# Kernel tuning notes

Measured on AMD Instinct MI355X. Metric: run time of the kernel, lower is better.

The kernel has to match this reference:

```python
import jax, jax.numpy as jnp
import numpy as np

N_NODES = 100_000
N_EDGES = 1_600_000
D_IN, D_HID, D_OUT = 256, 64, 32
NUM_PROP = 10
ALPHA = 0.1


def setup_inputs() -> dict:
    key = jax.random.key(0)
    ks = jax.random.split(key, 8)
    features = jax.random.normal(ks[0], (N_NODES, D_IN), dtype=jnp.float32)
    row = jax.random.randint(ks[1], (N_EDGES,), 0, N_NODES, dtype=jnp.int32)
    col = jax.random.randint(ks[2], (N_EDGES,), 0, N_NODES, dtype=jnp.int32)
    # positive edge weights (stand-in for symmetric-normalized adjacency values)
    edge_vals = jax.random.uniform(ks[3], (N_EDGES,), dtype=jnp.float32) / 16.0
    W1 = jax.random.normal(ks[4], (D_IN, D_HID), dtype=jnp.float32) / np.sqrt(D_IN)
    b1 = jnp.zeros((D_HID,), dtype=jnp.float32)
    W2 = jax.random.normal(ks[5], (D_HID, D_OUT), dtype=jnp.float32) / np.sqrt(D_HID)
    b2 = jnp.zeros((D_OUT,), dtype=jnp.float32)
    return {"features": features, "row": row, "col": col, "edge_vals": edge_vals,
            "W1": W1, "b1": b1, "W2": W2, "b2": b2}


def _spmm(row, col, vals, x):
    # COO sparse-dense matmul: out[r] += vals[e] * x[col[e]] for each edge e
    return jax.ops.segment_sum(vals[:, None] * x[col], row, num_segments=N_NODES)


def reference(features, row, col, edge_vals, W1, b1, W2, b2):
    # head_transform: 2-layer MLP
    x = jax.nn.relu(features @ W1 + b1) @ W2 + b2  # [N, D_OUT]
    x0 = x
    # APPNP propagation: x = (1-alpha) * (A @ x) + alpha * x0
    def body(_, x):
        return (1.0 - ALPHA) * _spmm(row, col, edge_vals, x) + ALPHA * x0
    x = jax.lax.fori_loop(0, NUM_PROP, body, x)
    return x
```

## Files before the change

kernel.cpp:

```cpp
#include <hip/hip_runtime.h>

#define N_NODES 100000
#define N_EDGES 1600000
#define D_IN    256
#define D_HID   64
#define D_OUT   32
#define NPROP   10

#define NBUCK 196
#define CHUNK 6080
#define NCHUNK ((N_EDGES + CHUNK - 1) / CHUNK)

typedef _Float16 half_t;
typedef _Float16 h8  __attribute__((ext_vector_type(8)));
typedef _Float16 h4  __attribute__((ext_vector_type(4)));
typedef float    f4v __attribute__((ext_vector_type(4)));

__global__ __launch_bounds__(256) void pack_kernel(
    const float* __restrict__ W1, const float* __restrict__ W2,
    half_t* __restrict__ W1T, half_t* __restrict__ W2T)
{
  int t = blockIdx.x * 256 + threadIdx.x;
  if (t < 64 * 256) { int n = t >> 8, k = t & 255; W1T[t] = (half_t)W1[k * 64 + n]; }
  if (t < 32 * 64)  { int n = t >> 6, k = t & 63;  W2T[t] = (half_t)W2[k * 32 + n]; }
}

#define HSTRIDE 72

__global__ __launch_bounds__(256, 4) void mlp_kernel(
    const float* __restrict__ F, const half_t* __restrict__ W1T,
    const float* __restrict__ b1, const half_t* __restrict__ W2T,
    const float* __restrict__ b2, half_t* __restrict__ x0h)
{
  __shared__ half_t h_lds[4 * 16 * HSTRIDE];
  __shared__ half_t out_lds[4 * 16 * 32];
  int t = threadIdx.x;
  int w = t >> 6, lane = t & 63;
  int m = lane & 15, q = lane >> 4;
  int gw = blockIdx.x * 4 + w;
  int node0 = gw * 16;
  if (node0 > N_NODES - 16) node0 = N_NODES - 16;

  f4v acc[4];
#pragma unroll
  for (int i = 0; i < 4; ++i) acc[i] = (f4v){0.f, 0.f, 0.f, 0.f};

  const float* ap = F + (size_t)(node0 + m) * D_IN + q * 8;

#pragma unroll
  for (int h = 0; h < 2; ++h) {
    h8 af[4];
#pragma unroll
    for (int s = 0; s < 4; ++s) {
      float4 f0 = *(const float4*)(ap + h * 128 + s * 32);
      float4 f1 = *(const float4*)(ap + h * 128 + s * 32 + 4);
      h8 a;
      a[0] = (_Float16)f0.x; a[1] = (_Float16)f0.y;
      a[2] = (_Float16)f0.z; a[3] = (_Float16)f0.w;
      a[4] = (_Float16)f1.x; a[5] = (_Float16)f1.y;
      a[6] = (_Float16)f1.z; a[7] = (_Float16)f1.w;
      af[s] = a;
    }
    const half_t* bp = W1T + (size_t)m * D_IN + h * 128 + q * 8;
#pragma unroll
    for (int s = 0; s < 4; ++s) {
      h8 b0 = *(const h8*)(bp + 0 * 16 * D_IN + s * 32);
      h8 b1v = *(const h8*)(bp + 1 * 16 * D_IN + s * 32);
      h8 b2v = *(const h8*)(bp + 2 * 16 * D_IN + s * 32);
      h8 b3v = *(const h8*)(bp + 3 * 16 * D_IN + s * 32);
      acc[0] = __builtin_amdgcn_mfma_f32_16x16x32_f16(af[s], b0, acc[0], 0, 0, 0);
      acc[1] = __builtin_amdgcn_mfma_f32_16x16x32_f16(af[s], b1v, acc[1], 0, 0, 0);
      acc[2] = __builtin_amdgcn_mfma_f32_16x16x32_f16(af[s], b2v, acc[2], 0, 0, 0);
      acc[3] = __builtin_amdgcn_mfma_f32_16x16x32_f16(af[s], b3v, acc[3], 0, 0, 0);
    }
  }

  half_t* hw = h_lds + w * 16 * HSTRIDE;
#pragma unroll
  for (int ht = 0; ht < 4; ++ht) {
    float bb = b1[ht * 16 + m];
#pragma unroll
    for (int i = 0; i < 4; ++i) {
      float hv = fmaxf(acc[ht][i] + bb, 0.f);
      hw[(q * 4 + i) * HSTRIDE + ht * 16 + m] = (half_t)hv;
    }
  }
  __syncthreads();

  f4v o0 = {0.f, 0.f, 0.f, 0.f}, o1 = {0.f, 0.f, 0.f, 0.f};
#pragma unroll
  for (int s = 0; s < 2; ++s) {
    h8 a = *(const h8*)(hw + m * HSTRIDE + s * 32 + q * 8);
    h8 bb0 = *(const h8*)(W2T + (size_t)m * D_HID + s * 32 + q * 8);
    h8 bb1 = *(const h8*)(W2T + (size_t)(16 + m) * D_HID + s * 32 + q * 8);
    o0 = __builtin_amdgcn_mfma_f32_16x16x32_f16(a, bb0, o0, 0, 0, 0);
    o1 = __builtin_amdgcn_mfma_f32_16x16x32_f16(a, bb1, o1, 0, 0, 0);
  }
  half_t* ow = out_lds + w * 16 * 32;
  {
    float c0 = b2[m], c1 = b2[16 + m];
#pragma unroll
    for (int i = 0; i < 4; ++i) {
      ow[(q * 4 + i) * 32 + m]      = (half_t)(o0[i] + c0);
      ow[(q * 4 + i) * 32 + 16 + m] = (half_t)(o1[i] + c1);
    }
  }
  __syncthreads();

  {
    int nl = lane >> 2, qq = lane & 3;
    *(int4*)(x0h + (size_t)(node0 + nl) * D_OUT + qq * 8) =
        *(const int4*)(ow + nl * 32 + qq * 8);
  }
}

__global__ __launch_bounds__(256) void bhist_kernel(
    const int* __restrict__ row, int* __restrict__ bcnt)
{
  __shared__ int lb[NBUCK];
  int t = threadIdx.x;
  for (int i = t; i < NBUCK; i += 256) lb[i] = 0;
  __syncthreads();
  int stride = gridDim.x * 256;
  for (int e = blockIdx.x * 256 + t; e < N_EDGES; e += stride)
    atomicAdd(&lb[row[e] >> 9], 1);
  __syncthreads();
  for (int i = t; i < NBUCK; i += 256)
    if (lb[i]) atomicAdd(&bcnt[i], lb[i]);
}

__global__ __launch_bounds__(256) void bscan_kernel(
    const int* __restrict__ bcnt, int* __restrict__ bbase, int* __restrict__ pbase)
{
  __shared__ int l1[256], l2[256];
  int t = threadIdx.x;
  int a = (t < NBUCK) ? bcnt[t] : 0;
  int r = (t < NBUCK) ? (((a + 3) & ~3) + 3 * 512) : 0;
  l1[t] = a; l2[t] = r;
  __syncthreads();
  for (int off = 1; off < 256; off <<= 1) {
    int x1 = (t >= off) ? l1[t - off] : 0;
    int x2 = (t >= off) ? l2[t - off] : 0;
    __syncthreads();
    l1[t] += x1; l2[t] += x2;
    __syncthreads();
  }
  if (t < NBUCK) { bbase[t] = l1[t] - a; pbase[t] = l2[t] - r; }
  if (t == NBUCK - 1) { bbase[NBUCK] = l1[t]; pbase[NBUCK] = l2[t]; }
}

__global__ __launch_bounds__(256) void bscatter_kernel(
    const int* __restrict__ row, const int* __restrict__ col,
    const float* __restrict__ vals, int* __restrict__ bfill,
    const int* __restrict__ bbase, int2* __restrict__ ebuck)
{
  __shared__ int2 img[CHUNK];
  __shared__ unsigned short sbk[CHUNK];
  __shared__ int cnt[NBUCK], base[NBUCK], gb[NBUCK], fil[NBUCK];
  __shared__ int ssc[256];
  int t = threadIdx.x;
  int e0 = blockIdx.x * CHUNK;
  int n = min(CHUNK, N_EDGES - e0);

  for (int i = t; i < NBUCK; i += 256) { cnt[i] = 0; fil[i] = 0; }
  __syncthreads();
  for (int i = t; i < n; i += 256) atomicAdd(&cnt[row[e0 + i] >> 9], 1);
  __syncthreads();
  int c = (t < NBUCK) ? cnt[t] : 0;
  ssc[t] = c;
  __syncthreads();
  for (int off = 1; off < 256; off <<= 1) {
    int add = (t >= off) ? ssc[t - off] : 0;
    __syncthreads();
    ssc[t] += add;
    __syncthreads();
  }
  if (t < NBUCK) {
    base[t] = ssc[t] - c;
    gb[t] = c ? atomicAdd(&bfill[t], c) : 0;
  }
  __syncthreads();
  for (int i = t; i < n; i += 256) {
    int r = row[e0 + i];
    int bk = r >> 9;
    int p = base[bk] + atomicAdd(&fil[bk], 1);
    img[p] = make_int2(col[e0 + i] | ((r & 511) << 17),
                       __float_as_int(vals[e0 + i]));
    sbk[p] = (unsigned short)bk;
  }
  __syncthreads();
  for (int i = t; i < n; i += 256) {
    int bk = sbk[i];
    ebuck[bbase[bk] + gb[bk] + (i - base[bk])] = img[i];
  }
}

__global__ __launch_bounds__(256) void bsort_kernel(
    const int* __restrict__ bbase, const int* __restrict__ pbase,
    const int2* __restrict__ ebuck, int2* __restrict__ epack,
    int* __restrict__ row_ptr)
{
  __shared__ int acnt[512], loff[513], lfill[512], ssc[256];
  int b = blockIdx.x, t = threadIdx.x;
  int r0 = b * 512;
  int nr = min(512, N_NODES - r0);
  int eb = bbase[b];
  int ne = bbase[b + 1] - eb;
  int pb = pbase[b];

  acnt[t] = 0; acnt[t + 256] = 0;
  lfill[t] = 0; lfill[t + 256] = 0;
  __syncthreads();
  for (int i = t; i < ne; i += 256)
    atomicAdd(&acnt[((unsigned)ebuck[eb + i].x) >> 17], 1);
  __syncthreads();
  int i0 = 2 * t, i1 = 2 * t + 1;
  int a0 = acnt[i0], a1 = acnt[i1];
  int p0 = (a0 + 3) & ~3, p1 = (a1 + 3) & ~3;
  int s = p0 + p1;
  ssc[t] = s;
  __syncthreads();
  for (int off = 1; off < 256; off <<= 1) {
    int add = (t >= off) ? ssc[t - off] : 0;
    __syncthreads();
    ssc[t] += add;
    __syncthreads();
  }
  int ex = ssc[t] - s;
  loff[i0] = ex;
  loff[i1] = ex + p0;
  if (t == 255) loff[512] = ssc[255];
  __syncthreads();
  int T = ssc[255];
  int slack = (pbase[b + 1] - pb) - T;
  int units = min(slack >> 2, nr);
  if (i0 < nr) row_ptr[r0 + i0] = pb + loff[i0] + 4 * min(i0, units);
  if (i1 < nr) row_ptr[r0 + i1] = pb + loff[i1] + 4 * min(i1, units);
  if (b == NBUCK - 1 && t == 0)
    row_ptr[N_NODES] = pb + loff[nr] + 4 * units;
  __syncthreads();
  for (int i = t; i < ne; i += 256) {
    int2 ed = ebuck[eb + i];
    int lr = ((unsigned)ed.x) >> 17;
    int cl = ed.x & 0x1FFFF;
    int p = loff[lr] + 4 * min(lr, units) + atomicAdd(&lfill[lr], 1);
    epack[pb + p] = make_int2(cl, ed.y);
  }
  __syncthreads();
  for (int i = t; i < nr; i += 256) {
    int a = acnt[i];
    int size_i = ((a + 3) & ~3) + 4 * (i < units);
    int st = loff[i] + 4 * min(i, units);
    for (int p = st + a; p < st + size_i; ++p)
      epack[pb + p] = make_int2(0, 0);
  }
}

__global__ __launch_bounds__(256) void spmm_kernel(
    const int* __restrict__ rp, const int2* __restrict__ ep,
    const half_t* __restrict__ xin, const half_t* __restrict__ x0h,
    half_t* __restrict__ xout, float* __restrict__ fout, int last)
{
  int gt = blockIdx.x * 256 + threadIdx.x;
  int r = gt >> 3;
  int c4 = (gt & 7) * 4;
  if (r >= N_NODES) return;
  int e0 = rp[r], e1 = rp[r + 1];

  float acc[4] = {0.f, 0.f, 0.f, 0.f};
  for (int e = e0; e < e1; e += 4) {
    int2 p0 = ep[e];
    int2 p1 = ep[e + 1];
    int2 p2 = ep[e + 2];
    int2 p3 = ep[e + 3];
    h4 g0 = *(const h4*)(xin + (size_t)p0.x * D_OUT + c4);
    h4 g1 = *(const h4*)(xin + (size_t)p1.x * D_OUT + c4);
    h4 g2 = *(const h4*)(xin + (size_t)p2.x * D_OUT + c4);
    h4 g3 = *(const h4*)(xin + (size_t)p3.x * D_OUT + c4);
    float v0 = __int_as_float(p0.y);
    float v1 = __int_as_float(p1.y);
    float v2 = __int_as_float(p2.y);
    float v3 = __int_as_float(p3.y);
#pragma unroll
    for (int j = 0; j < 4; ++j) {
      acc[j] = fmaf(v0, (float)g0[j], acc[j]);
      acc[j] = fmaf(v1, (float)g1[j], acc[j]);
      acc[j] = fmaf(v2, (float)g2[j], acc[j]);
      acc[j] = fmaf(v3, (float)g3[j], acc[j]);
    }
  }

  h4 x0v = *(const h4*)(x0h + (size_t)r * D_OUT + c4);
  if (last) {
    float4 o;
    o.x = 0.9f * acc[0] + 0.1f * (float)x0v[0];
    o.y = 0.9f * acc[1] + 0.1f * (float)x0v[1];
    o.z = 0.9f * acc[2] + 0.1f * (float)x0v[2];
    o.w = 0.9f * acc[3] + 0.1f * (float)x0v[3];
    *(float4*)(fout + (size_t)r * D_OUT + c4) = o;
  } else {
    h4 o;
#pragma unroll
    for (int j = 0; j < 4; ++j)
      o[j] = (half_t)(0.9f * acc[j] + 0.1f * (float)x0v[j]);
    *(h4*)(xout + (size_t)r * D_OUT + c4) = o;
  }
}

extern "C" void kernel_launch(void* const* d_in, const int* in_sizes, int n_in,
                              void* d_out, int out_size, void* d_ws, size_t ws_size,
                              hipStream_t stream) {
  const float* F     = (const float*)d_in[0];
  const int*   row   = (const int*)  d_in[1];
  const int*   col   = (const int*)  d_in[2];
  const float* evals = (const float*)d_in[3];
  const float* W1    = (const float*)d_in[4];
  const float* b1    = (const float*)d_in[5];
  const float* W2    = (const float*)d_in[6];
  const float* b2    = (const float*)d_in[7];
  float* out = (float*)d_out;

  char* w = (char*)d_ws;
  half_t* x0h    = (half_t*)(w);
  half_t* P      = (half_t*)(w +  6400000);
  half_t* Q      = (half_t*)(w + 12800000);
  int2*   ebuck  = (int2*)  (w +  6400000);
  int2*   epack  = (int2*)  (w + 19200000);
  int*   row_ptr = (int*)   (w + 34600192);
  int*   bcnt    = (int*)   (w + 35000576);
  int*   bfill   = (int*)   (w + 35001600);
  int*   bbase   = (int*)   (w + 35002624);
  int*   pbase   = (int*)   (w + 35003648);
  half_t* W1T    = (half_t*)(w + 35004672);
  half_t* W2T    = (half_t*)(w + 35037440);

  pack_kernel<<<64, 256, 0, stream>>>(W1, W2, W1T, W2T);
  mlp_kernel<<<(N_NODES / 16 + 3) / 4, 256, 0, stream>>>(F, W1T, b1, W2T, b2, x0h);

  hipMemsetAsync(bcnt, 0, 2048, stream);
  bhist_kernel<<<640, 256, 0, stream>>>(row, bcnt);
  bscan_kernel<<<1, 256, 0, stream>>>(bcnt, bbase, pbase);
  bscatter_kernel<<<NCHUNK, 256, 0, stream>>>(row, col, evals, bfill, bbase, ebuck);
  bsort_kernel<<<NBUCK, 256, 0, stream>>>(bbase, pbase, ebuck, epack, row_ptr);

  const int grid_spmm = (N_NODES * 8 + 255) / 256;
  for (int i = 0; i < NPROP; ++i) {
    const half_t* xin = (i == 0) ? x0h : ((i & 1) ? P : Q);
    half_t* xout = (i & 1) ? Q : P;
    int last = (i == NPROP - 1);
    spmm_kernel<<<grid_spmm, 256, 0, stream>>>(
        row_ptr, epack, xin, x0h, xout, out, last);
  }
}
```

Measured before the change: 532.1 us.

## Sort rows by degree within buckets and vectorize edge loads in SpMM

```diff
diff --git a/kernel.cpp b/kernel.cpp
--- a/kernel.cpp
+++ b/kernel.cpp
@@ -198,9 +198,10 @@
 __global__ __launch_bounds__(256) void bsort_kernel(
     const int* __restrict__ bbase, const int* __restrict__ pbase,
     const int2* __restrict__ ebuck, int2* __restrict__ epack,
-    int* __restrict__ row_ptr)
+    int* __restrict__ row_ptr, int* __restrict__ ridx)
 {
   __shared__ int acnt[512], loff[513], lfill[512], ssc[256];
+  __shared__ int dh[512], dfil[512];
   int b = blockIdx.x, t = threadIdx.x;
   int r0 = b * 512;
   int nr = min(512, N_NODES - r0);
@@ -254,33 +255,63 @@
     for (int p = st + a; p < st + size_i; ++p)
       epack[pb + p] = make_int2(0, 0);
   }
+  dh[t] = 0; dh[t + 256] = 0;
+  dfil[t] = 0; dfil[t + 256] = 0;
+  __syncthreads();
+  if (i0 < nr) atomicAdd(&dh[min(acnt[i0], 511)], 1);
+  if (i1 < nr) atomicAdd(&dh[min(acnt[i1], 511)], 1);
+  __syncthreads();
+  int d0 = dh[i0], d1 = dh[i1];
+  int sd = d0 + d1;
+  ssc[t] = sd;
+  __syncthreads();
+  for (int off = 1; off < 256; off <<= 1) {
+    int add = (t >= off) ? ssc[t - off] : 0;
+    __syncthreads();
+    ssc[t] += add;
+    __syncthreads();
+  }
+  int exd = ssc[t] - sd;
+  dh[i0] = exd;
+  dh[i1] = exd + d0;
+  __syncthreads();
+  if (i0 < nr) {
+    int d = min(acnt[i0], 511);
+    int p = dh[d] + atomicAdd(&dfil[d], 1);
+    ridx[r0 + p] = r0 + i0;
+  }
+  if (i1 < nr) {
+    int d = min(acnt[i1], 511);
+    int p = dh[d] + atomicAdd(&dfil[d], 1);
+    ridx[r0 + p] = r0 + i1;
+  }
 }
 
 __global__ __launch_bounds__(256) void spmm_kernel(
-    const int* __restrict__ rp, const int2* __restrict__ ep,
+    const int* __restrict__ rp, const int* __restrict__ ridx,
+    const int2* __restrict__ ep,
     const half_t* __restrict__ xin, const half_t* __restrict__ x0h,
     half_t* __restrict__ xout, float* __restrict__ fout, int last)
 {
   int gt = blockIdx.x * 256 + threadIdx.x;
-  int r = gt >> 3;
+  int rh = gt >> 3;
   int c4 = (gt & 7) * 4;
-  if (r >= N_NODES) return;
+  if (rh >= N_NODES) return;
+  int r = ridx[rh];
   int e0 = rp[r], e1 = rp[r + 1];
 
   float acc[4] = {0.f, 0.f, 0.f, 0.f};
   for (int e = e0; e < e1; e += 4) {
-    int2 p0 = ep[e];
-    int2 p1 = ep[e + 1];
-    int2 p2 = ep[e + 2];
-    int2 p3 = ep[e + 3];
-    h4 g0 = *(const h4*)(xin + (size_t)p0.x * D_OUT + c4);
-    h4 g1 = *(const h4*)(xin + (size_t)p1.x * D_OUT + c4);
-    h4 g2 = *(const h4*)(xin + (size_t)p2.x * D_OUT + c4);
-    h4 g3 = *(const h4*)(xin + (size_t)p3.x * D_OUT + c4);
-    float v0 = __int_as_float(p0.y);
-    float v1 = __int_as_float(p1.y);
-    float v2 = __int_as_float(p2.y);
-    float v3 = __int_as_float(p3.y);
+    int4 q0 = *(const int4*)(ep + e);
+    int4 q1 = *(const int4*)(ep + e + 2);
+    h4 g0 = *(const h4*)(xin + (size_t)q0.x * D_OUT + c4);
+    h4 g1 = *(const h4*)(xin + (size_t)q0.z * D_OUT + c4);
+    h4 g2 = *(const h4*)(xin + (size_t)q1.x * D_OUT + c4);
+    h4 g3 = *(const h4*)(xin + (size_t)q1.z * D_OUT + c4);
+    float v0 = __int_as_float(q0.y);
+    float v1 = __int_as_float(q0.w);
+    float v2 = __int_as_float(q1.y);
+    float v3 = __int_as_float(q1.w);
 #pragma unroll
     for (int j = 0; j < 4; ++j) {
       acc[j] = fmaf(v0, (float)g0[j], acc[j]);
@@ -333,6 +364,7 @@
   int*   pbase   = (int*)   (w + 35003648);
   half_t* W1T    = (half_t*)(w + 35004672);
   half_t* W2T    = (half_t*)(w + 35037440);
+  int*   ridx    = (int*)   (w + 35041536);
 
   pack_kernel<<<64, 256, 0, stream>>>(W1, W2, W1T, W2T);
   mlp_kernel<<<(N_NODES / 16 + 3) / 4, 256, 0, stream>>>(F, W1T, b1, W2T, b2, x0h);
@@ -341,7 +373,7 @@
   bhist_kernel<<<640, 256, 0, stream>>>(row, bcnt);
   bscan_kernel<<<1, 256, 0, stream>>>(bcnt, bbase, pbase);
   bscatter_kernel<<<NCHUNK, 256, 0, stream>>>(row, col, evals, bfill, bbase, ebuck);
-  bsort_kernel<<<NBUCK, 256, 0, stream>>>(bbase, pbase, ebuck, epack, row_ptr);
+  bsort_kernel<<<NBUCK, 256, 0, stream>>>(bbase, pbase, ebuck, epack, row_ptr, ridx);
 
   const int grid_spmm = (N_NODES * 8 + 255) / 256;
   for (int i = 0; i < NPROP; ++i) {
@@ -349,6 +381,6 @@
     half_t* xout = (i & 1) ? Q : P;
     int last = (i == NPROP - 1);
     spmm_kernel<<<grid_spmm, 256, 0, stream>>>(
-        row_ptr, epack, xin, x0h, xout, out, last);
-  }
-}
+        row_ptr, ridx, epack, xin, x0h, xout, out, last);
+  }
+}
```

New measurement: 582.5 us. 1.09x slower.

## Prefetch edge packets and use nontemporal loads/stores in SpMM; batch MLP feature loads

Applied to the files above, without the earlier changes.

```diff
diff --git a/kernel.cpp b/kernel.cpp
--- a/kernel.cpp
+++ b/kernel.cpp
@@ -15,6 +15,15 @@
 typedef _Float16 h8  __attribute__((ext_vector_type(8)));
 typedef _Float16 h4  __attribute__((ext_vector_type(4)));
 typedef float    f4v __attribute__((ext_vector_type(4)));
+typedef int      i4v __attribute__((ext_vector_type(4)));
+typedef int      i2v __attribute__((ext_vector_type(2)));
+
+static __device__ __forceinline__ h4 bc_h4(i2v v) {
+  h4 r; __builtin_memcpy(&r, &v, 8); return r;
+}
+static __device__ __forceinline__ i2v bc_i2(h4 v) {
+  i2v r; __builtin_memcpy(&r, &v, 8); return r;
+}
 
 __global__ __launch_bounds__(256) void pack_kernel(
     const float* __restrict__ W1, const float* __restrict__ W2,
@@ -27,7 +36,7 @@
 
 #define HSTRIDE 72
 
-__global__ __launch_bounds__(256, 4) void mlp_kernel(
+__global__ __launch_bounds__(256, 2) void mlp_kernel(
     const float* __restrict__ F, const half_t* __restrict__ W1T,
     const float* __restrict__ b1, const half_t* __restrict__ W2T,
     const float* __restrict__ b2, half_t* __restrict__ x0h)
@@ -41,38 +50,40 @@
   int node0 = gw * 16;
   if (node0 > N_NODES - 16) node0 = N_NODES - 16;
 
+  const float* ap = F + (size_t)(node0 + m) * D_IN + q * 8;
+  float4 fr[16];
+#pragma unroll
+  for (int s = 0; s < 8; ++s) {
+    fr[2 * s]     = *(const float4*)(ap + s * 32);
+    fr[2 * s + 1] = *(const float4*)(ap + s * 32 + 4);
+  }
+
+  h8 af[8];
+#pragma unroll
+  for (int s = 0; s < 8; ++s) {
+    float4 f0 = fr[2 * s], f1 = fr[2 * s + 1];
+    h8 a;
+    a[0] = (_Float16)f0.x; a[1] = (_Float16)f0.y;
+    a[2] = (_Float16)f0.z; a[3] = (_Float16)f0.w;
+    a[4] = (_Float16)f1.x; a[5] = (_Float16)f1.y;
+    a[6] = (_Float16)f1.z; a[7] = (_Float16)f1.w;
+    af[s] = a;
+  }
+
   f4v acc[4];
 #pragma unroll
   for (int i = 0; i < 4; ++i) acc[i] = (f4v){0.f, 0.f, 0.f, 0.f};
-
-  const float* ap = F + (size_t)(node0 + m) * D_IN + q * 8;
-
-#pragma unroll
-  for (int h = 0; h < 2; ++h) {
-    h8 af[4];
-#pragma unroll
-    for (int s = 0; s < 4; ++s) {
-      float4 f0 = *(const float4*)(ap + h * 128 + s * 32);
-      float4 f1 = *(const float4*)(ap + h * 128 + s * 32 + 4);
-      h8 a;
-      a[0] = (_Float16)f0.x; a[1] = (_Float16)f0.y;
-      a[2] = (_Float16)f0.z; a[3] = (_Float16)f0.w;
-      a[4] = (_Float16)f1.x; a[5] = (_Float16)f1.y;
-      a[6] = (_Float16)f1.z; a[7] = (_Float16)f1.w;
-      af[s] = a;
-    }
-    const half_t* bp = W1T + (size_t)m * D_IN + h * 128 + q * 8;
-#pragma unroll
-    for (int s = 0; s < 4; ++s) {
-      h8 b0 = *(const h8*)(bp + 0 * 16 * D_IN + s * 32);
-      h8 b1v = *(const h8*)(bp + 1 * 16 * D_IN + s * 32);
-      h8 b2v = *(const h8*)(bp + 2 * 16 * D_IN + s * 32);
-      h8 b3v = *(const h8*)(bp + 3 * 16 * D_IN + s * 32);
-      acc[0] = __builtin_amdgcn_mfma_f32_16x16x32_f16(af[s], b0, acc[0], 0, 0, 0);
-      acc[1] = __builtin_amdgcn_mfma_f32_16x16x32_f16(af[s], b1v, acc[1], 0, 0, 0);
-      acc[2] = __builtin_amdgcn_mfma_f32_16x16x32_f16(af[s], b2v, acc[2], 0, 0, 0);
-      acc[3] = __builtin_amdgcn_mfma_f32_16x16x32_f16(af[s], b3v, acc[3], 0, 0, 0);
-    }
+  const half_t* bp = W1T + (size_t)m * D_IN + q * 8;
+#pragma unroll
+  for (int s = 0; s < 8; ++s) {
+    h8 b0 = *(const h8*)(bp + 0 * 16 * D_IN + s * 32);
+    h8 b1v = *(const h8*)(bp + 1 * 16 * D_IN + s * 32);
+    h8 b2v = *(const h8*)(bp + 2 * 16 * D_IN + s * 32);
+    h8 b3v = *(const h8*)(bp + 3 * 16 * D_IN + s * 32);
+    acc[0] = __builtin_amdgcn_mfma_f32_16x16x32_f16(af[s], b0, acc[0], 0, 0, 0);
+    acc[1] = __builtin_amdgcn_mfma_f32_16x16x32_f16(af[s], b1v, acc[1], 0, 0, 0);
+    acc[2] = __builtin_amdgcn_mfma_f32_16x16x32_f16(af[s], b2v, acc[2], 0, 0, 0);
+    acc[3] = __builtin_amdgcn_mfma_f32_16x16x32_f16(af[s], b3v, acc[3], 0, 0, 0);
   }
 
   half_t* hw = h_lds + w * 16 * HSTRIDE;
@@ -267,20 +278,31 @@
   if (r >= N_NODES) return;
   int e0 = rp[r], e1 = rp[r + 1];
 
+  i2v x0b = __builtin_nontemporal_load(
+      (const i2v*)(x0h + (size_t)r * D_OUT + c4));
+  h4 x0v = bc_h4(x0b);
+
   float acc[4] = {0.f, 0.f, 0.f, 0.f};
-  for (int e = e0; e < e1; e += 4) {
-    int2 p0 = ep[e];
-    int2 p1 = ep[e + 1];
-    int2 p2 = ep[e + 2];
-    int2 p3 = ep[e + 3];
-    h4 g0 = *(const h4*)(xin + (size_t)p0.x * D_OUT + c4);
-    h4 g1 = *(const h4*)(xin + (size_t)p1.x * D_OUT + c4);
-    h4 g2 = *(const h4*)(xin + (size_t)p2.x * D_OUT + c4);
-    h4 g3 = *(const h4*)(xin + (size_t)p3.x * D_OUT + c4);
-    float v0 = __int_as_float(p0.y);
-    float v1 = __int_as_float(p1.y);
-    float v2 = __int_as_float(p2.y);
-    float v3 = __int_as_float(p3.y);
+  i4v q0 = {0, 0, 0, 0}, q1 = {0, 0, 0, 0};
+  if (e0 < e1) {
+    q0 = __builtin_nontemporal_load((const i4v*)(ep + e0));
+    q1 = __builtin_nontemporal_load((const i4v*)(ep + e0 + 2));
+  }
+  for (int e = e0; e < e1; ) {
+    i4v c0 = q0, c1 = q1;
+    int en = e + 4;
+    if (en < e1) {
+      q0 = __builtin_nontemporal_load((const i4v*)(ep + en));
+      q1 = __builtin_nontemporal_load((const i4v*)(ep + en + 2));
+    }
+    h4 g0 = *(const h4*)(xin + (size_t)c0[0] * D_OUT + c4);
+    h4 g1 = *(const h4*)(xin + (size_t)c0[2] * D_OUT + c4);
+    h4 g2 = *(const h4*)(xin + (size_t)c1[0] * D_OUT + c4);
+    h4 g3 = *(const h4*)(xin + (size_t)c1[2] * D_OUT + c4);
+    float v0 = __int_as_float(c0[1]);
+    float v1 = __int_as_float(c0[3]);
+    float v2 = __int_as_float(c1[1]);
+    float v3 = __int_as_float(c1[3]);
 #pragma unroll
     for (int j = 0; j < 4; ++j) {
       acc[j] = fmaf(v0, (float)g0[j], acc[j]);
@@ -288,22 +310,22 @@
       acc[j] = fmaf(v2, (float)g2[j], acc[j]);
       acc[j] = fmaf(v3, (float)g3[j], acc[j]);
     }
-  }
-
-  h4 x0v = *(const h4*)(x0h + (size_t)r * D_OUT + c4);
+    e = en;
+  }
+
   if (last) {
-    float4 o;
-    o.x = 0.9f * acc[0] + 0.1f * (float)x0v[0];
-    o.y = 0.9f * acc[1] + 0.1f * (float)x0v[1];
-    o.z = 0.9f * acc[2] + 0.1f * (float)x0v[2];
-    o.w = 0.9f * acc[3] + 0.1f * (float)x0v[3];
-    *(float4*)(fout + (size_t)r * D_OUT + c4) = o;
+    f4v o;
+    o[0] = 0.9f * acc[0] + 0.1f * (float)x0v[0];
+    o[1] = 0.9f * acc[1] + 0.1f * (float)x0v[1];
+    o[2] = 0.9f * acc[2] + 0.1f * (float)x0v[2];
+    o[3] = 0.9f * acc[3] + 0.1f * (float)x0v[3];
+    __builtin_nontemporal_store(o, (f4v*)(fout + (size_t)r * D_OUT + c4));
   } else {
     h4 o;
 #pragma unroll
     for (int j = 0; j < 4; ++j)
       o[j] = (half_t)(0.9f * acc[j] + 0.1f * (float)x0v[j]);
-    *(h4*)(xout + (size_t)r * D_OUT + c4) = o;
+    __builtin_nontemporal_store(bc_i2(o), (i2v*)(xout + (size_t)r * D_OUT + c4));
   }
 }
 
```

Result: slower. 590.7 us (+11.0%).
